# Kernel optimization log

Hardware: AMD Instinct MI355X
Metric: run time of the kernel (lower is better)

The kernel has to match this reference:

```python
import jax, jax.numpy as jnp
import numpy as np

N, SD, VD, LD = 8192, 512, 4096, 768
TAU = 0.5
K = 6    # topk over stru->mm similarity
K2 = 6   # topk2 over mm->mm similarity
BN_EPS = 1e-5
LRELU_SLOPE = 0.01


def _mlp_bn(x, W1, b1, W2, b2, gamma, beta):
    # Linear -> LeakyReLU -> Linear -> BatchNorm1d (training mode, batch stats)
    h = x @ W1 + b1
    h = jnp.where(h >= 0, h, LRELU_SLOPE * h)
    h = h @ W2 + b2
    mu = h.mean(axis=0)
    var = h.var(axis=0)  # biased variance, as torch BN uses for normalization
    return (h - mu) / jnp.sqrt(var + BN_EPS) * gamma + beta


def _cossim(x, y):
    xn = x / (jnp.linalg.norm(x, axis=-1, keepdims=True) + 1e-12)
    yn = y / (jnp.linalg.norm(y, axis=-1, keepdims=True) + 1e-12)
    return xn @ yn.T


def _neibor_mnce_v2(stru, mm):
    sm = jnp.exp(_cossim(stru, mm) / TAU)   # [N, N]
    mmd = _cossim(mm, mm)                    # [N, N]
    _, maxSM = jax.lax.top_k(sm, K)          # [N, K]
    rows = jnp.arange(stru.shape[0])[:, None]
    pos = []
    for i in range(K):  # fixed small loop over topk columns (as in original)
        idx = maxSM[:, i]                         # [N]
        _, mm_idx = jax.lax.top_k(mmd[idx], K2)   # gather rows then topk -> [N, K2]
        pos.append(sm[rows, mm_idx])              # [N, K2]
    pos = jnp.concatenate(pos, axis=-1)           # [N, K*K2]
    return jnp.mean(-jnp.log(pos.sum(-1) / sm.sum(-1)))


def setup_inputs() -> dict:
    key = jax.random.key(0)
    ks = jax.random.split(key, 11)
    d = {
        'stru_feats': jax.random.normal(ks[0], (N, SD), jnp.float32),
        'visu_feats': jax.random.normal(ks[1], (N, VD), jnp.float32),
        'ling_feats': jax.random.normal(ks[2], (N, LD), jnp.float32),
        # fusion_l_vl params
        'Wl1': jax.random.normal(ks[3], (LD, SD), jnp.float32) / np.sqrt(LD),
        'bl1': jnp.zeros((SD,), jnp.float32),
        'Wl2': jax.random.normal(ks[4], (SD, SD), jnp.float32) / np.sqrt(SD),
        'bl2': jnp.zeros((SD,), jnp.float32),
        'gl': jnp.ones((SD,), jnp.float32),
        'betal': jnp.zeros((SD,), jnp.float32),
        # fusion_v_vl params
        'Wv1': jax.random.normal(ks[5], (VD, SD), jnp.float32) / np.sqrt(VD),
        'bv1': jnp.zeros((SD,), jnp.float32),
        'Wv2': jax.random.normal(ks[6], (SD, SD), jnp.float32) / np.sqrt(SD),
        'bv2': jnp.zeros((SD,), jnp.float32),
        'gv': jnp.ones((SD,), jnp.float32),
        'betav': jnp.zeros((SD,), jnp.float32),
    }
    return d


def reference(stru_feats, visu_feats, ling_feats,
              Wl1, bl1, Wl2, bl2, gl, betal,
              Wv1, bv1, Wv2, bv2, gv, betav):
    ling = _mlp_bn(ling_feats, Wl1, bl1, Wl2, bl2, gl, betal)
    visu = _mlp_bn(visu_feats, Wv1, bv1, Wv2, bv2, gv, betav)
    loss_sl = _neibor_mnce_v2(stru_feats, ling)
    loss_sv = _neibor_mnce_v2(stru_feats, visu)
    return (loss_sl + loss_sv, ling, visu)
```

## Files before the change

kernel.cpp:

```cpp
#include <hip/hip_runtime.h>
#include <hip/hip_bf16.h>
#include <math.h>

typedef __bf16 bf16;
typedef __attribute__((ext_vector_type(8))) __bf16 bf16x8;
typedef __attribute__((ext_vector_type(4))) float floatx4;

static_assert(sizeof(bf16x8) == 16, "bf16x8 must be 16B");

__device__ __forceinline__ void gld16(bf16* lds, const bf16* g) {
  __builtin_amdgcn_global_load_lds((const __attribute__((address_space(1))) void*)g,
                                   (__attribute__((address_space(3))) void*)lds, 16, 0, 0);
}

__global__ void row_normalize_kernel(const float* __restrict__ x, bf16* __restrict__ out) {
  __shared__ float red[256];
  int row = blockIdx.x;
  int t = threadIdx.x;
  float v0 = x[(size_t)row * 512 + t];
  float v1 = x[(size_t)row * 512 + t + 256];
  red[t] = v0 * v0 + v1 * v1;
  __syncthreads();
  for (int d = 128; d > 0; d >>= 1) {
    if (t < d) red[t] += red[t + d];
    __syncthreads();
  }
  float scale = 1.0f / (sqrtf(red[0]) + 1e-12f);
  out[(size_t)row * 512 + t] = (bf16)(v0 * scale);
  out[(size_t)row * 512 + t + 256] = (bf16)(v1 * scale);
}

__global__ void cast_bf16_kernel(const float* __restrict__ x, bf16* __restrict__ out, long n) {
  long i = ((long)blockIdx.x * blockDim.x + threadIdx.x) * 8;
  long stride = (long)gridDim.x * blockDim.x * 8;
  for (; i < n; i += stride) {
    floatx4 a = *(const floatx4*)(x + i);
    floatx4 b = *(const floatx4*)(x + i + 4);
    bf16x8 v;
#pragma unroll
    for (int e = 0; e < 4; ++e) v[e] = (bf16)a[e];
#pragma unroll
    for (int e = 0; e < 4; ++e) v[e + 4] = (bf16)b[e];
    *(bf16x8*)(out + i) = v;
  }
}

__global__ void transpose_cast_kernel(const float* __restrict__ W, bf16* __restrict__ Wt, int K) {
  __shared__ float t[64][65];
  int k0 = blockIdx.x * 64;
  int n0 = blockIdx.y * 64;
#pragma unroll
  for (int m = 0; m < 16; ++m) {
    int kk = (threadIdx.x >> 6) + m * 4;
    int nn = threadIdx.x & 63;
    t[kk][nn] = W[(size_t)(k0 + kk) * 512 + n0 + nn];
  }
  __syncthreads();
#pragma unroll
  for (int m = 0; m < 16; ++m) {
    int nn = (threadIdx.x >> 6) + m * 4;
    int kk = threadIdx.x & 63;
    Wt[(size_t)(n0 + nn) * K + k0 + kk] = (bf16)t[kk][nn];
  }
}

__global__ void bn_stats_kernel(const float* __restrict__ h, float* __restrict__ colsum,
                                float* __restrict__ colsumsq) {
  int col = threadIdx.x;
  int r0 = blockIdx.x * 32;
  float s = 0.f, s2 = 0.f;
  for (int r = r0; r < r0 + 32; ++r) {
    float v = h[(size_t)r * 512 + col];
    s += v;
    s2 += v * v;
  }
  atomicAdd(&colsum[col], s);
  atomicAdd(&colsumsq[col], s2);
}

__global__ void bn_apply_kernel(const float* __restrict__ h, const float* __restrict__ colsum,
                                const float* __restrict__ colsumsq, const float* __restrict__ gamma,
                                const float* __restrict__ beta, float* __restrict__ mm_out,
                                bf16* __restrict__ mmn) {
  __shared__ float red[512];
  int row = blockIdx.x, col = threadIdx.x;
  float mean = colsum[col] * (1.0f / 8192.0f);
  float var = colsumsq[col] * (1.0f / 8192.0f) - mean * mean;
  float inv = rsqrtf(var + 1e-5f);
  float y = (h[(size_t)row * 512 + col] - mean) * inv * gamma[col] + beta[col];
  mm_out[(size_t)row * 512 + col] = y;
  red[col] = y * y;
  __syncthreads();
  for (int d = 256; d > 0; d >>= 1) {
    if (col < d) red[col] += red[col + d];
    __syncthreads();
  }
  float scale = 1.0f / (sqrtf(red[0]) + 1e-12f);
  mmn[(size_t)row * 512 + col] = (bf16)(y * scale);
}

template <int MODE, bool AF32>
__launch_bounds__(256, 2) __global__
void gemm_nt_kernel(const void* __restrict__ Av, const bf16* __restrict__ B,
                    const float* __restrict__ bias, bf16* __restrict__ out_bf,
                    float* __restrict__ out_f, int K) {
  __shared__ __align__(16) bf16 As[2][128][64];
  __shared__ __align__(16) bf16 Bs[2][64][64];

  const int tid = threadIdx.x;
  const int lane = tid & 63;
  const int wave = tid >> 6;
  const int q = lane >> 4;
  const int ml = lane & 15;
  const int row0 = blockIdx.x * 128;
  const int col0 = blockIdx.y * 64;

  const float* Af = (const float*)Av;
  const bf16* Ab = (const bf16*)Av;

  floatx4 acc[2][4];
#pragma unroll
  for (int g = 0; g < 2; ++g)
#pragma unroll
    for (int f = 0; f < 4; ++f) acc[g][f] = (floatx4)0.0f;

  const int nsteps = K >> 6;

  if constexpr (!AF32) {
    const int grow = lane >> 3;
    const int gch = (lane & 7) ^ grow;

    auto stageA = [&](int s, int b) {
      const int kt = s << 6;
#pragma unroll
      for (int m = 0; m < 4; ++m) {
        const int rb = m * 32 + wave * 8;
        gld16(&As[b][rb][0], Ab + (size_t)(row0 + rb + grow) * K + kt + gch * 8);
      }
    };
    auto stageB = [&](int s, int b) {
      const int kt = s << 6;
#pragma unroll
      for (int m = 0; m < 2; ++m) {
        const int rb = m * 32 + wave * 8;
        gld16(&Bs[b][rb][0], B + (size_t)(col0 + rb + grow) * K + kt + gch * 8);
      }
    };

    stageA(0, 0);
    stageB(0, 0);
    for (int s = 0; s < nsteps; ++s) {
      const int b = s & 1;
      __syncthreads();
      if (s + 1 < nsteps) {
        stageA(s + 1, b ^ 1);
        stageB(s + 1, b ^ 1);
      }
      __builtin_amdgcn_s_setprio(1);
#pragma unroll
      for (int kh = 0; kh < 2; ++kh) {
        const int slot = ((q + kh * 4) ^ (ml & 7)) * 8;
        bf16x8 a0 = *(const bf16x8*)&As[b][wave * 32 + ml][slot];
        bf16x8 a1 = *(const bf16x8*)&As[b][wave * 32 + 16 + ml][slot];
#pragma unroll
        for (int f = 0; f < 4; ++f) {
          bf16x8 bb = *(const bf16x8*)&Bs[b][f * 16 + ml][slot];
          acc[0][f] = __builtin_amdgcn_mfma_f32_16x16x32_bf16(a0, bb, acc[0][f], 0, 0, 0);
          acc[1][f] = __builtin_amdgcn_mfma_f32_16x16x32_bf16(a1, bb, acc[1][f], 0, 0, 0);
        }
      }
      __builtin_amdgcn_s_setprio(0);
    }
  } else {
    const int sr = tid >> 3;
    const int sc = tid & 7;
    for (int s = 0; s < nsteps; ++s) {
      const int kt = s << 6;
      __syncthreads();
#pragma unroll
      for (int m = 0; m < 4; ++m) {
        int r = sr + m * 32;
        const float* pp = Af + (size_t)(row0 + r) * K + kt + sc * 8;
        bf16x8 v;
#pragma unroll
        for (int e = 0; e < 8; ++e) v[e] = (bf16)pp[e];
        *(bf16x8*)&As[0][r][(sc ^ (r & 7)) * 8] = v;
      }
#pragma unroll
      for (int m = 0; m < 2; ++m) {
        int r = sr + m * 32;
        *(bf16x8*)&Bs[0][r][(sc ^ (r & 7)) * 8] =
            *(const bf16x8*)(B + (size_t)(col0 + r) * K + kt + sc * 8);
      }
      __syncthreads();
#pragma unroll
      for (int kh = 0; kh < 2; ++kh) {
        const int slot = ((q + kh * 4) ^ (ml & 7)) * 8;
        bf16x8 a0 = *(const bf16x8*)&As[0][wave * 32 + ml][slot];
        bf16x8 a1 = *(const bf16x8*)&As[0][wave * 32 + 16 + ml][slot];
#pragma unroll
        for (int f = 0; f < 4; ++f) {
          bf16x8 bb = *(const bf16x8*)&Bs[0][f * 16 + ml][slot];
          acc[0][f] = __builtin_amdgcn_mfma_f32_16x16x32_bf16(a0, bb, acc[0][f], 0, 0, 0);
          acc[1][f] = __builtin_amdgcn_mfma_f32_16x16x32_bf16(a1, bb, acc[1][f], 0, 0, 0);
        }
      }
    }
  }

#pragma unroll
  for (int f = 0; f < 4; ++f) {
    int colg = col0 + f * 16 + ml;
    float bv = bias[colg];
#pragma unroll
    for (int g = 0; g < 2; ++g)
#pragma unroll
      for (int i = 0; i < 4; ++i) {
        int rowg = row0 + wave * 32 + g * 16 + q * 4 + i;
        float v = acc[g][f][i] + bv;
        if constexpr (MODE == 0) {
          v = v >= 0.f ? v : 0.01f * v;
          out_bf[(size_t)rowg * 512 + colg] = (bf16)v;
        } else {
          out_f[(size_t)rowg * 512 + colg] = v;
        }
      }
  }
}

__device__ __forceinline__ unsigned pack_key(float v, int col) {
  unsigned u = __float_as_uint(v);
  u = (u & 0x80000000u) ? ~u : (u | 0x80000000u);
  return (u & 0xFFFFE000u) | (unsigned)(8191 - col);
}

#define NPARTS 8

__launch_bounds__(256, 2) __global__
void topk_sm_fused_kernel(const bf16* __restrict__ Amm, const bf16* __restrict__ Ast,
                          const bf16* __restrict__ B, unsigned* __restrict__ keys_mm,
                          unsigned* __restrict__ keys_sm, float* __restrict__ rowsum_part) {
  __shared__ __align__(16) bf16 Bs[2][64][128];

  const int tid = threadIdx.x;
  const int lane = tid & 63;
  const int wave = tid >> 6;
  const int q = lane >> 4;
  const int ml = lane & 15;
  const int row0 = blockIdx.x * 64;
  const int part = blockIdx.y;

  const int strw = wave * 4 + (lane >> 4);
  const int gch = (lane & 15) ^ strw;

  bf16x8 afr[2][16];
#pragma unroll
  for (int g = 0; g < 2; ++g) {
    const bf16* ap = (g == 0 ? Amm : Ast) + (size_t)(row0 + wave * 16 + ml) * 512 + q * 8;
#pragma unroll
    for (int s = 0; s < 16; ++s) afr[g][s] = *(const bf16x8*)(ap + s * 32);
  }

  unsigned p6[2][4][6];
#pragma unroll
  for (int g = 0; g < 2; ++g)
#pragma unroll
    for (int i = 0; i < 4; ++i)
#pragma unroll
      for (int j = 0; j < 6; ++j) p6[g][i][j] = 0u;
  float srow[4] = {0.f, 0.f, 0.f, 0.f};

  auto stage = [&](int u, int b) {
    const bf16* bp =
        B + (size_t)(part * 1024 + (u >> 2) * 64 + strw) * 512 + (u & 3) * 128 + gch * 8;
#pragma unroll
    for (int m = 0; m < 4; ++m)
      gld16(&Bs[b][wave * 4 + m * 16][0], bp + (size_t)m * 16 * 512);
  };

  stage(0, 0);

  for (int ct = 0; ct < 16; ++ct) {
    const int col0 = part * 1024 + ct * 64;
    floatx4 acc[2][4];
#pragma unroll
    for (int g = 0; g < 2; ++g)
#pragma unroll
      for (int f = 0; f < 4; ++f) acc[g][f] = (floatx4)0.0f;

#pragma unroll
    for (int kt4 = 0; kt4 < 4; ++kt4) {
      const int t = ct * 4 + kt4;
      __syncthreads();
      if (t < 63) stage(t + 1, (t + 1) & 1);
      __builtin_amdgcn_s_setprio(1);
#pragma unroll
      for (int kk2 = 0; kk2 < 4; ++kk2) {
#pragma unroll
        for (int f = 0; f < 4; ++f) {
          const int sc2 = (kk2 * 4 + q) ^ ml;
          bf16x8 b = *(const bf16x8*)&Bs[t & 1][f * 16 + ml][sc2 * 8];
          acc[0][f] = __builtin_amdgcn_mfma_f32_16x16x32_bf16(afr[0][kt4 * 4 + kk2], b, acc[0][f], 0, 0, 0);
          acc[1][f] = __builtin_amdgcn_mfma_f32_16x16x32_bf16(afr[1][kt4 * 4 + kk2], b, acc[1][f], 0, 0, 0);
        }
      }
      __builtin_amdgcn_s_setprio(0);
    }

#pragma unroll
    for (int i = 0; i < 4; ++i) {
      float s = 0.f;
#pragma unroll
      for (int f = 0; f < 4; ++f) s += __expf(2.0f * acc[1][f][i]);
      srow[i] += s;
#pragma unroll
      for (int g = 0; g < 2; ++g)
#pragma unroll
        for (int f = 0; f < 4; ++f) {
          unsigned key = pack_key(acc[g][f][i], col0 + f * 16 + ml);
          if (key > p6[g][i][5]) {
#pragma unroll
            for (int j = 5; j >= 1; --j) {
              bool ap = key > p6[g][i][j - 1];
              unsigned keep = (key > p6[g][i][j]) ? key : p6[g][i][j];
              p6[g][i][j] = ap ? p6[g][i][j - 1] : keep;
            }
            if (key > p6[g][i][0]) p6[g][i][0] = key;
          }
        }
    }
  }

#pragma unroll
  for (int i = 0; i < 4; ++i) {
    const int lrow = wave * 16 + q * 4 + i;
    {
      float s = srow[i];
      s += __shfl_xor(s, 1);
      s += __shfl_xor(s, 2);
      s += __shfl_xor(s, 4);
      s += __shfl_xor(s, 8);
      if (ml == 0) rowsum_part[(size_t)(row0 + lrow) * NPARTS + part] = s;
    }
#pragma unroll
    for (int g = 0; g < 2; ++g) {
      unsigned* dk = g ? keys_sm : keys_mm;
      const size_t o = ((size_t)(row0 + lrow) * NPARTS + part) * 6;
#pragma unroll
      for (int k = 0; k < 6; ++k) {
        unsigned mk = p6[g][i][0];
#pragma unroll
        for (int d = 1; d < 16; d <<= 1) {
          unsigned ok = (unsigned)__shfl_xor((int)mk, d);
          if (ok > mk) mk = ok;
        }
        if (ml == 0) dk[o + k] = mk;
        if (p6[g][i][0] == mk) {
#pragma unroll
          for (int j = 0; j < 5; ++j) p6[g][i][j] = p6[g][i][j + 1];
          p6[g][i][5] = 0u;
        }
      }
    }
  }
}

__global__ void merge_top6_kernel(const unsigned* __restrict__ part_keys,
                                  int* __restrict__ out_idx,
                                  const float* __restrict__ rowsum_part, float* __restrict__ rowsum,
                                  int do_rowsum) {
  int row = blockIdx.x * blockDim.x + threadIdx.x;
  if (row >= 8192) return;
  unsigned best[6] = {0u, 0u, 0u, 0u, 0u, 0u};
  for (int p = 0; p < NPARTS; ++p) {
#pragma unroll
    for (int c = 0; c < 6; ++c) {
      unsigned k = part_keys[((size_t)row * NPARTS + p) * 6 + c];
      if (k > best[5]) {
#pragma unroll
        for (int j = 5; j >= 1; --j) {
          bool ap = k > best[j - 1];
          unsigned keep = (k > best[j]) ? k : best[j];
          best[j] = ap ? best[j - 1] : keep;
        }
        if (k > best[0]) best[0] = k;
      }
    }
  }
#pragma unroll
  for (int j = 0; j < 6; ++j) out_idx[row * 6 + j] = 8191 - (int)(best[j] & 0x1FFFu);
  if (do_rowsum) {
    float s = 0.f;
    for (int p = 0; p < NPARTS; ++p) s += rowsum_part[(size_t)row * NPARTS + p];
    rowsum[row] = s;
  }
}

__global__ void loss_kernel(const bf16* __restrict__ strun, const bf16* __restrict__ mmn,
                            const int* __restrict__ top6, const int* __restrict__ nbr,
                            const float* __restrict__ rowsum, float* __restrict__ out0) {
  int w = (int)((blockIdx.x * blockDim.x + threadIdx.x) >> 6);
  int lane = threadIdx.x & 63;
  if (w >= 8192) return;
  bf16x8 sv = *(const bf16x8*)(strun + (size_t)w * 512 + lane * 8);
  float sf[8];
#pragma unroll
  for (int e = 0; e < 8; ++e) sf[e] = (float)sv[e];
  float pos = 0.f;
  for (int k = 0; k < 6; ++k) {
    int j = top6[w * 6 + k];
#pragma unroll
    for (int l = 0; l < 6; ++l) {
      int m = nbr[j * 6 + l];
      bf16x8 mv = *(const bf16x8*)(mmn + (size_t)m * 512 + lane * 8);
      float d = 0.f;
#pragma unroll
      for (int e = 0; e < 8; ++e) d += sf[e] * (float)mv[e];
      d += __shfl_xor(d, 1);
      d += __shfl_xor(d, 2);
      d += __shfl_xor(d, 4);
      d += __shfl_xor(d, 8);
      d += __shfl_xor(d, 16);
      d += __shfl_xor(d, 32);
      pos += __expf(2.0f * d);
    }
  }
  if (lane == 0) {
    float loss_r = logf(rowsum[w]) - logf(pos);
    atomicAdd(out0, loss_r * (1.0f / 8192.0f));
  }
}

extern "C" void kernel_launch(void* const* d_in, const int* in_sizes, int n_in, void* d_out,
                              int out_size, void* d_ws, size_t ws_size, hipStream_t stream) {
  const float* stru = (const float*)d_in[0];
  const float* visu = (const float*)d_in[1];
  const float* ling = (const float*)d_in[2];
  const float* Wl1 = (const float*)d_in[3];
  const float* bl1 = (const float*)d_in[4];
  const float* Wl2 = (const float*)d_in[5];
  const float* bl2 = (const float*)d_in[6];
  const float* gl = (const float*)d_in[7];
  const float* betal = (const float*)d_in[8];
  const float* Wv1 = (const float*)d_in[9];
  const float* bv1 = (const float*)d_in[10];
  const float* Wv2 = (const float*)d_in[11];
  const float* bv2 = (const float*)d_in[12];
  const float* gv = (const float*)d_in[13];
  const float* betav = (const float*)d_in[14];
  float* out = (float*)d_out;

  char* p = (char*)d_ws;
  auto alloc = [&](size_t bytes) {
    char* r = p;
    p += (bytes + 255) & ~(size_t)255;
    return r;
  };
  bf16* strun = (bf16*)alloc((size_t)8192 * 512 * 2);
  bf16* W1t = (bf16*)alloc((size_t)512 * 4096 * 2);
  bf16* W2t = (bf16*)alloc((size_t)512 * 512 * 2);
  bf16* H1 = (bf16*)alloc((size_t)8192 * 512 * 2);
  float* H2 = (float*)alloc((size_t)8192 * 512 * 4);
  bf16* mmn = (bf16*)alloc((size_t)8192 * 512 * 2);
  float* colsum = (float*)alloc(512 * 4);
  float* colsumsq = (float*)alloc(512 * 4);
  float* rowsum_part = (float*)alloc((size_t)8192 * NPARTS * 4);
  float* rowsum = (float*)alloc((size_t)8192 * 4);
  unsigned* keys_mm = (unsigned*)alloc((size_t)8192 * NPARTS * 6 * 4);
  unsigned* keys_sm = (unsigned*)alloc((size_t)8192 * NPARTS * 6 * 4);
  int* nbr = (int*)alloc((size_t)8192 * 6 * 4);
  int* top6 = (int*)alloc((size_t)8192 * 6 * 4);

  size_t xb_bytes = (size_t)8192 * 4096 * 2;
  size_t used = (size_t)(p - (char*)d_ws);
  bf16* Xb = nullptr;
  if (used + xb_bytes <= ws_size) Xb = (bf16*)alloc(xb_bytes);

  hipMemsetAsync(d_out, 0, 4, stream);
  row_normalize_kernel<<<8192, 256, 0, stream>>>(stru, strun);

  for (int br = 0; br < 2; ++br) {
    const float* X = (br == 0) ? ling : visu;
    int Kin = (br == 0) ? 768 : 4096;
    const float* W1 = (br == 0) ? Wl1 : Wv1;
    const float* b1 = (br == 0) ? bl1 : bv1;
    const float* W2 = (br == 0) ? Wl2 : Wv2;
    const float* b2 = (br == 0) ? bl2 : bv2;
    const float* g = (br == 0) ? gl : gv;
    const float* bet = (br == 0) ? betal : betav;
    float* mm_out = out + 1 + (size_t)br * 8192 * 512;

    transpose_cast_kernel<<<dim3(Kin / 64, 8), 256, 0, stream>>>(W1, W1t, Kin);
    transpose_cast_kernel<<<dim3(8, 8), 256, 0, stream>>>(W2, W2t, 512);

    if (Xb) {
      cast_bf16_kernel<<<2048, 256, 0, stream>>>(X, Xb, (long)8192 * Kin);
      gemm_nt_kernel<0, false><<<dim3(64, 8), 256, 0, stream>>>(
          Xb, W1t, b1, H1, nullptr, Kin);
    } else {
      gemm_nt_kernel<0, true><<<dim3(64, 8), 256, 0, stream>>>(
          X, W1t, b1, H1, nullptr, Kin);
    }
    gemm_nt_kernel<1, false><<<dim3(64, 8), 256, 0, stream>>>(
        H1, W2t, b2, nullptr, H2, 512);

    hipMemsetAsync(colsum, 0, 512 * 4, stream);
    hipMemsetAsync(colsumsq, 0, 512 * 4, stream);
    bn_stats_kernel<<<256, 512, 0, stream>>>(H2, colsum, colsumsq);
    bn_apply_kernel<<<8192, 512, 0, stream>>>(H2, colsum, colsumsq, g, bet, mm_out, mmn);

    topk_sm_fused_kernel<<<dim3(128, NPARTS), 256, 0, stream>>>(
        mmn, strun, mmn, keys_mm, keys_sm, rowsum_part);
    merge_top6_kernel<<<32, 256, 0, stream>>>(keys_mm, nbr, nullptr, nullptr, 0);
    merge_top6_kernel<<<32, 256, 0, stream>>>(keys_sm, top6, rowsum_part, rowsum, 1);

    loss_kernel<<<2048, 256, 0, stream>>>(strun, mmn, top6, nbr, rowsum, out);
  }
}
```

Baseline: 1.071 ms.

## Triple-buffer LDS staging with prefetch distance two and vmcnt-based waits

Both the bf16 GEMM and the fused top-k similarity kernel go from double-buffered to triple-buffered LDS tiles. Global-to-LDS loads are issued two steps ahead. The full __syncthreads is replaced by an explicit s_waitcnt vmcnt plus a raw s_barrier, so loads for the next tile can stay in flight. This aims to hide global memory latency behind MFMA work. In exchange it uses more LDS per block, which may lower occupancy, and the hand-counted vmcnt values must match the number of loads issued per stage.

```diff
diff --git a/kernel.cpp b/kernel.cpp
--- a/kernel.cpp
+++ b/kernel.cpp
@@ -12,6 +12,9 @@
   __builtin_amdgcn_global_load_lds((const __attribute__((address_space(1))) void*)g,
                                    (__attribute__((address_space(3))) void*)lds, 16, 0, 0);
 }
+
+#define VMCNT(N) asm volatile("s_waitcnt vmcnt(" #N ")" ::: "memory")
+#define RAW_BARRIER() asm volatile("s_barrier" ::: "memory")
 
 __global__ void row_normalize_kernel(const float* __restrict__ x, bf16* __restrict__ out) {
   __shared__ float red[256];
@@ -104,8 +107,8 @@
 void gemm_nt_kernel(const void* __restrict__ Av, const bf16* __restrict__ B,
                     const float* __restrict__ bias, bf16* __restrict__ out_bf,
                     float* __restrict__ out_f, int K) {
-  __shared__ __align__(16) bf16 As[2][128][64];
-  __shared__ __align__(16) bf16 Bs[2][64][64];
+  __shared__ __align__(16) bf16 As[3][128][64];
+  __shared__ __align__(16) bf16 Bs[3][64][64];
 
   const int tid = threadIdx.x;
   const int lane = tid & 63;
@@ -130,16 +133,13 @@
     const int grow = lane >> 3;
     const int gch = (lane & 7) ^ grow;
 
-    auto stageA = [&](int s, int b) {
+    auto stageAB = [&](int s, int b) {
       const int kt = s << 6;
 #pragma unroll
       for (int m = 0; m < 4; ++m) {
         const int rb = m * 32 + wave * 8;
         gld16(&As[b][rb][0], Ab + (size_t)(row0 + rb + grow) * K + kt + gch * 8);
       }
-    };
-    auto stageB = [&](int s, int b) {
-      const int kt = s << 6;
 #pragma unroll
       for (int m = 0; m < 2; ++m) {
         const int rb = m * 32 + wave * 8;
@@ -147,29 +147,33 @@
       }
     };
 
-    stageA(0, 0);
-    stageB(0, 0);
+    stageAB(0, 0);
+    stageAB(1, 1);
+    int cur = 0;
     for (int s = 0; s < nsteps; ++s) {
-      const int b = s & 1;
-      __syncthreads();
-      if (s + 1 < nsteps) {
-        stageA(s + 1, b ^ 1);
-        stageB(s + 1, b ^ 1);
-      }
+      if (s == nsteps - 1) { VMCNT(0); } else { VMCNT(6); }
+      __builtin_amdgcn_sched_barrier(0);
+      RAW_BARRIER();
+      __builtin_amdgcn_sched_barrier(0);
+      int nb = cur + 2;
+      if (nb >= 3) nb -= 3;
+      if (s + 2 < nsteps) stageAB(s + 2, nb);
       __builtin_amdgcn_s_setprio(1);
 #pragma unroll
       for (int kh = 0; kh < 2; ++kh) {
         const int slot = ((q + kh * 4) ^ (ml & 7)) * 8;
-        bf16x8 a0 = *(const bf16x8*)&As[b][wave * 32 + ml][slot];
-        bf16x8 a1 = *(const bf16x8*)&As[b][wave * 32 + 16 + ml][slot];
+        bf16x8 a0 = *(const bf16x8*)&As[cur][wave * 32 + ml][slot];
+        bf16x8 a1 = *(const bf16x8*)&As[cur][wave * 32 + 16 + ml][slot];
 #pragma unroll
         for (int f = 0; f < 4; ++f) {
-          bf16x8 bb = *(const bf16x8*)&Bs[b][f * 16 + ml][slot];
+          bf16x8 bb = *(const bf16x8*)&Bs[cur][f * 16 + ml][slot];
           acc[0][f] = __builtin_amdgcn_mfma_f32_16x16x32_bf16(a0, bb, acc[0][f], 0, 0, 0);
           acc[1][f] = __builtin_amdgcn_mfma_f32_16x16x32_bf16(a1, bb, acc[1][f], 0, 0, 0);
         }
       }
       __builtin_amdgcn_s_setprio(0);
+      cur = cur + 1;
+      if (cur >= 3) cur -= 3;
     }
   } else {
     const int sr = tid >> 3;
@@ -240,7 +244,7 @@
 void topk_sm_fused_kernel(const bf16* __restrict__ Amm, const bf16* __restrict__ Ast,
                           const bf16* __restrict__ B, unsigned* __restrict__ keys_mm,
                           unsigned* __restrict__ keys_sm, float* __restrict__ rowsum_part) {
-  __shared__ __align__(16) bf16 Bs[2][64][128];
+  __shared__ __align__(16) bf16 Bs[3][64][128];
 
   const int tid = threadIdx.x;
   const int lane = tid & 63;
@@ -279,6 +283,8 @@
   };
 
   stage(0, 0);
+  stage(1, 1);
+  int cur = 0;
 
   for (int ct = 0; ct < 16; ++ct) {
     const int col0 = part * 1024 + ct * 64;
@@ -291,20 +297,33 @@
 #pragma unroll
     for (int kt4 = 0; kt4 < 4; ++kt4) {
       const int t = ct * 4 + kt4;
-      __syncthreads();
-      if (t < 63) stage(t + 1, (t + 1) & 1);
+      if (kt4 == 3) {
+        if (ct == 15) { VMCNT(0); } else { VMCNT(4); }
+      } else {
+        VMCNT(4);
+      }
+      __builtin_amdgcn_sched_barrier(0);
+      RAW_BARRIER();
+      __builtin_amdgcn_sched_barrier(0);
+      {
+        int nb = cur + 2;
+        if (nb >= 3) nb -= 3;
+        if (ct < 15 || kt4 < 2) stage(t + 2, nb);
+      }
       __builtin_amdgcn_s_setprio(1);
 #pragma unroll
       for (int kk2 = 0; kk2 < 4; ++kk2) {
 #pragma unroll
         for (int f = 0; f < 4; ++f) {
           const int sc2 = (kk2 * 4 + q) ^ ml;
-          bf16x8 b = *(const bf16x8*)&Bs[t & 1][f * 16 + ml][sc2 * 8];
+          bf16x8 b = *(const bf16x8*)&Bs[cur][f * 16 + ml][sc2 * 8];
           acc[0][f] = __builtin_amdgcn_mfma_f32_16x16x32_bf16(afr[0][kt4 * 4 + kk2], b, acc[0][f], 0, 0, 0);
           acc[1][f] = __builtin_amdgcn_mfma_f32_16x16x32_bf16(afr[1][kt4 * 4 + kk2], b, acc[1][f], 0, 0, 0);
         }
       }
       __builtin_amdgcn_s_setprio(0);
+      cur = cur + 1;
+      if (cur >= 3) cur -= 3;
     }
 
 #pragma unroll
```

Measured after the change: 1.081 ms. Within noise of the previous version (+0.9%).
